# Performance work log

Hardware: AMD Instinct MI355X
Metric: run time of the kernel (lower is better)

The kernel has to match this reference:

```python
import jax, jax.numpy as jnp
import numpy as np

DIST_THR = 0.2
CONTACT_TGT = 0.1
ALPHA = 0.01
HUBER_DELTA = 0.01
W_BCE = 0.5
W_DIST = 1.0
EPS = 1e-06


def setup_inputs() -> dict:
    key = jax.random.key(0)
    k1, k2, k3, k4 = jax.random.split(key, 4)
    BT, Vh, Vo = 16, 6890, 2048
    return {
        "human_verts": jax.random.uniform(k1, (BT, Vh, 3), dtype=jnp.float32),
        "object_verts": jax.random.uniform(k2, (BT, Vo, 3), dtype=jnp.float32),
        "gt_human_verts": jax.random.uniform(k3, (BT, Vh, 3), dtype=jnp.float32),
        "gt_object_verts": jax.random.uniform(k4, (BT, Vo, 3), dtype=jnp.float32),
    }


def _min_cdist(A, B):
    # A:[BT,NA,3], B:[BT,NB,3] -> min Euclidean distance over B: [BT,NA]
    aa = jnp.sum(A * A, axis=-1)               # [BT,NA]
    bb = jnp.sum(B * B, axis=-1)               # [BT,NB]
    ab = jnp.einsum("bnd,bmd->bnm", A, B)      # [BT,NA,NB]
    d2 = aa[:, :, None] + bb[:, None, :] - 2.0 * ab
    d = jnp.sqrt(jnp.maximum(d2, 0.0))
    return jnp.min(d, axis=-1)


def _bce_balanced(p, target):
    p = jnp.clip(p, 1e-06, 1.0 - 1e-06)
    pos = jnp.sum(target)
    neg = target.size - pos
    pos_w = (neg + EPS) / (pos + EPS)
    w = jnp.where(target > 0.5, pos_w, 1.0)
    loss = -(target * jnp.log(p) + (1.0 - target) * jnp.log(1.0 - p))
    return jnp.mean(w * loss)


def _masked_huber(over, mask):
    m = (mask > 0.5).astype(over.dtype)
    ax = jnp.abs(over)
    hub = jnp.where(ax < HUBER_DELTA, 0.5 * ax * ax / HUBER_DELTA, ax - 0.5 * HUBER_DELTA)
    cnt = jnp.sum(m)
    s = jnp.sum(hub * m)
    return jnp.where(cnt > 0, s / jnp.maximum(cnt, 1.0), 0.0)


def reference(human_verts, object_verts, gt_human_verts, gt_object_verts):
    dmin_h = _min_cdist(human_verts, object_verts)      # [BT,Vh]
    dmin_o = _min_cdist(object_verts, human_verts)      # [BT,Vo]
    dmin_h_gt = _min_cdist(gt_human_verts, gt_object_verts)
    dmin_o_gt = _min_cdist(gt_object_verts, gt_human_verts)
    gt_mask_h = (dmin_h_gt < DIST_THR).astype(jnp.float32)
    gt_mask_o = (dmin_o_gt < DIST_THR).astype(jnp.float32)

    inv_alpha = 1.0 / max(ALPHA, 1e-08)
    p_h = jax.nn.sigmoid((DIST_THR - dmin_h) * inv_alpha)
    p_o = jax.nn.sigmoid((DIST_THR - dmin_o) * inv_alpha)
    L_bce = 0.5 * (_bce_balanced(p_h, gt_mask_h) + _bce_balanced(p_o, gt_mask_o))

    over_h = jnp.maximum(dmin_h - CONTACT_TGT, 0.0)
    over_o = jnp.maximum(dmin_o - CONTACT_TGT, 0.0)
    L_dist = _masked_huber(over_h, gt_mask_h) + _masked_huber(over_o, gt_mask_o)

    return W_BCE * L_bce + W_DIST * L_dist
```

## Files before the change

kernel.cpp:

```cpp
#include <hip/hip_runtime.h>
#include <math.h>


#define BT 16
#define VH 6890
#define VO 2048
#define NH (BT * VH)
#define NO (BT * VO)
#define RBLK1 54
#define RBLK2 16
#define NT1 64
#define NT2 216
#define NPROB 32
#define NBLK1 (NPROB * RBLK1)
#define NBLK2 (NPROB * RBLK2)

typedef __attribute__((ext_vector_type(8))) short          short8;
typedef __attribute__((ext_vector_type(8))) unsigned short ushort8;

__device__ __forceinline__ unsigned short bf16_rne(float f) {
    const unsigned int u = __float_as_uint(f);
    return (unsigned short)((u + 0x7FFFu + ((u >> 16) & 1u)) >> 16);
}
__device__ __forceinline__ float bf16_tof(unsigned short h) {
    return __uint_as_float(((unsigned int)h) << 16);
}

#define CLOB_B0 "v40","v41","v42","v43","v44","v45","v46","v47", \
                "v48","v49","v50","v51","v52","v53","v54","v55", \
                "v56","v57","v58","v59","v60","v61","v62","v63", \
                "v64","v65","v66","v67","v68","v69","v70","v71"
#define CLOB_B1 "v72","v73","v74","v75","v76","v77","v78","v79", \
                "v80","v81","v82","v83","v84","v85","v86","v87", \
                "v88","v89","v90","v91","v92","v93","v94","v95", \
                "v96","v97","v98","v99","v100","v101","v102","v103"

#define MFMA_B0(b0, b1) \
    asm volatile("v_mfma_f32_32x32x16_bf16 v[40:55], %0, %1, 0\n\t" \
                 "v_mfma_f32_32x32x16_bf16 v[56:71], %0, %2, 0" \
                 :: "v"(a8), "v"(b0), "v"(b1) : CLOB_B0)
#define MFMA_B1(b0, b1) \
    asm volatile("v_mfma_f32_32x32x16_bf16 v[72:87], %0, %1, 0\n\t" \
                 "v_mfma_f32_32x32x16_bf16 v[88:103], %0, %2, 0" \
                 :: "v"(a8), "v"(b0), "v"(b1) : CLOB_B1)

#define RED_B0() \
    asm volatile( \
        "v_min3_f32 %0, %0, v40, v56\n\t"  "v_min3_f32 %1, %1, v41, v57\n\t" \
        "v_min3_f32 %2, %2, v42, v58\n\t"  "v_min3_f32 %3, %3, v43, v59\n\t" \
        "v_min3_f32 %4, %4, v44, v60\n\t"  "v_min3_f32 %5, %5, v45, v61\n\t" \
        "v_min3_f32 %6, %6, v46, v62\n\t"  "v_min3_f32 %7, %7, v47, v63\n\t" \
        "v_min3_f32 %8, %8, v48, v64\n\t"  "v_min3_f32 %9, %9, v49, v65\n\t" \
        "v_min3_f32 %10, %10, v50, v66\n\t" "v_min3_f32 %11, %11, v51, v67\n\t" \
        "v_min3_f32 %12, %12, v52, v68\n\t" "v_min3_f32 %13, %13, v53, v69\n\t" \
        "v_min3_f32 %14, %14, v54, v70\n\t" "v_min3_f32 %15, %15, v55, v71" \
        : "+v"(rm[0]), "+v"(rm[1]), "+v"(rm[2]),  "+v"(rm[3]), \
          "+v"(rm[4]), "+v"(rm[5]), "+v"(rm[6]),  "+v"(rm[7]), \
          "+v"(rm[8]), "+v"(rm[9]), "+v"(rm[10]), "+v"(rm[11]), \
          "+v"(rm[12]),"+v"(rm[13]),"+v"(rm[14]), "+v"(rm[15]))
#define RED_B1() \
    asm volatile( \
        "v_min3_f32 %0, %0, v72, v88\n\t"  "v_min3_f32 %1, %1, v73, v89\n\t" \
        "v_min3_f32 %2, %2, v74, v90\n\t"  "v_min3_f32 %3, %3, v75, v91\n\t" \
        "v_min3_f32 %4, %4, v76, v92\n\t"  "v_min3_f32 %5, %5, v77, v93\n\t" \
        "v_min3_f32 %6, %6, v78, v94\n\t"  "v_min3_f32 %7, %7, v79, v95\n\t" \
        "v_min3_f32 %8, %8, v80, v96\n\t"  "v_min3_f32 %9, %9, v81, v97\n\t" \
        "v_min3_f32 %10, %10, v82, v98\n\t" "v_min3_f32 %11, %11, v83, v99\n\t" \
        "v_min3_f32 %12, %12, v84, v100\n\t" "v_min3_f32 %13, %13, v85, v101\n\t" \
        "v_min3_f32 %14, %14, v86, v102\n\t" "v_min3_f32 %15, %15, v87, v103" \
        : "+v"(rm[0]), "+v"(rm[1]), "+v"(rm[2]),  "+v"(rm[3]), \
          "+v"(rm[4]), "+v"(rm[5]), "+v"(rm[6]),  "+v"(rm[7]), \
          "+v"(rm[8]), "+v"(rm[9]), "+v"(rm[10]), "+v"(rm[11]), \
          "+v"(rm[12]),"+v"(rm[13]),"+v"(rm[14]), "+v"(rm[15]))

__global__ __launch_bounds__(256)
void prep_kernel(const float* __restrict__ hv,  const float* __restrict__ ov,
                 const float* __restrict__ ghv, const float* __restrict__ gov,
                 unsigned short* __restrict__ BfragO, unsigned short* __restrict__ BfragH,
                 unsigned int* __restrict__ acc)
{
    const int t = blockIdx.x * 256 + threadIdx.x;
    if (t < 16) acc[t] = 0u;

    const unsigned short one = 0x3F80;
    if (t < 65536) {
        const int col = t & 2047;
        const int bt  = (t >> 11) & 15;
        const int pg  = t >> 15;
        const float* B = (pg ? gov : ov) + ((size_t)bt * VO + col) * 3;
        const float bx = B[0], by = B[1], bz = B[2];
        const float m2x = -2.f * bx, m2y = -2.f * by, m2z = -2.f * bz;
        const float bb  = fmaf(bx, bx, fmaf(by, by, bz * bz));
        const unsigned short hx = bf16_rne(m2x), hy = bf16_rne(m2y), hz = bf16_rne(m2z);
        const unsigned short lx = bf16_rne(m2x - bf16_tof(hx));
        const unsigned short ly = bf16_rne(m2y - bf16_tof(hy));
        const unsigned short lz = bf16_rne(m2z - bf16_tof(hz));
        const unsigned short bh = bf16_rne(bb);
        const unsigned short bl = bf16_rne(bb - bf16_tof(bh));
        const int prob = pg * 16 + bt;
        unsigned short* d0 = BfragO +
            ((size_t)((prob * NT1 + (col >> 5)) * 64 + (col & 31))) * 8;
        const ushort8 w0 = {hx, hy, hz, hx, hy, hz, one, one};
        const ushort8 w1 = {lx, ly, lz, lx, ly, lz, bh, bl};
        *(ushort8*)d0         = w0;
        *(ushort8*)(d0 + 256) = w1;
    } else {
        const int t2   = t - 65536;
        const int col  = t2 % 6912;
        const int prob = t2 / 6912;
        const int pg = prob >> 4, bt = prob & 15;
        ushort8 w0, w1;
        if (col < VH) {
            const float* B = (pg ? ghv : hv) + ((size_t)bt * VH + col) * 3;
            const float bx = B[0], by = B[1], bz = B[2];
            const float m2x = -2.f * bx, m2y = -2.f * by, m2z = -2.f * bz;
            const float bb  = fmaf(bx, bx, fmaf(by, by, bz * bz));
            const unsigned short hx = bf16_rne(m2x), hy = bf16_rne(m2y), hz = bf16_rne(m2z);
            const unsigned short lx = bf16_rne(m2x - bf16_tof(hx));
            const unsigned short ly = bf16_rne(m2y - bf16_tof(hy));
            const unsigned short lz = bf16_rne(m2z - bf16_tof(hz));
            const unsigned short bh = bf16_rne(bb);
            const unsigned short bl = bf16_rne(bb - bf16_tof(bh));
            w0 = (ushort8){hx, hy, hz, hx, hy, hz, one, one};
            w1 = (ushort8){lx, ly, lz, lx, ly, lz, bh, bl};
        } else {
            const unsigned short big = bf16_rne(1.0e36f);
            w0 = (ushort8){0, 0, 0, 0, 0, 0, one, one};
            w1 = (ushort8){0, 0, 0, 0, 0, 0, big, 0};
        }
        unsigned short* d0 = BfragH +
            ((size_t)((prob * NT2 + (col >> 5)) * 64 + (col & 31))) * 8;
        *(ushort8*)d0         = w0;
        *(ushort8*)(d0 + 256) = w1;
    }
}

__global__ __launch_bounds__(256)
void mindist_mfma(const float* __restrict__ hv,  const float* __restrict__ ov,
                  const float* __restrict__ ghv, const float* __restrict__ gov,
                  const unsigned short* __restrict__ BfragO,
                  const unsigned short* __restrict__ BfragH,
                  float* __restrict__ rowm,
                  float* __restrict__ objm)
{
    const int tid  = threadIdx.x;
    const int lane = tid & 63;
    const int wave = tid >> 6;
    const int b    = blockIdx.x;

    const float* A;
    const short8* bls;
    float* out;
    int pairs, nA, row0;

    if (b < NBLK1) {
        const int prob = b / RBLK1, rblk = b - prob * RBLK1;
        const int pg = prob >> 4, bt = prob & 15;
        A    = (pg ? ghv : hv) + (size_t)bt * VH * 3;
        bls  = (const short8*)BfragO + (size_t)prob * (NT1 * 64);
        out  = rowm + (size_t)prob * VH;
        pairs = NT1 / 2; nA = VH; row0 = rblk * 128 + wave * 32;
    } else {
        const int b2 = b - NBLK1;
        const int prob = b2 >> 4, rblk = b2 & 15;
        const int pg = prob >> 4, bt = prob & 15;
        A    = (pg ? gov : ov) + (size_t)bt * VO * 3;
        bls  = (const short8*)BfragH + (size_t)prob * (NT2 * 64);
        out  = objm + (size_t)prob * 2048;
        pairs = NT2 / 2; nA = VO; row0 = rblk * 128 + wave * 32;
    }

    const int r = row0 + (lane & 31);
    float x, y, z;
    if (r < nA) { x = A[3*r]; y = A[3*r+1]; z = A[3*r+2]; }
    else        { x = 1.0e4f; y = 0.f;      z = 0.f; }
    const float aa = fmaf(x, x, fmaf(y, y, z * z));
    const unsigned short ahx = bf16_rne(x), ahy = bf16_rne(y), ahz = bf16_rne(z);
    const unsigned short alx = bf16_rne(x - bf16_tof(ahx));
    const unsigned short aly = bf16_rne(y - bf16_tof(ahy));
    const unsigned short alz = bf16_rne(z - bf16_tof(ahz));
    const unsigned short aah = bf16_rne(aa);
    const unsigned short aal = bf16_rne(aa - bf16_tof(aah));
    const int g = lane >> 5;
    ushort8 a8u;
    a8u[0] = ahx; a8u[1] = ahy; a8u[2] = ahz;
    a8u[3] = alx; a8u[4] = aly; a8u[5] = alz;
    a8u[6] = g ? (unsigned short)0x3F80 : aah;
    a8u[7] = g ? (unsigned short)0x3F80 : aal;
    const short8 a8 = (short8)a8u;

#define LD(jt) bls[(jt) * 64 + lane]
    float rm[16];
#pragma unroll
    for (int i = 0; i < 16; ++i) rm[i] = 3.0e38f;

    short8 bE0 = LD(0), bE1 = LD(1);
    MFMA_B0(bE0, bE1);
    short8 bO0 = LD(2), bO1 = LD(3);

    for (int s = 1; s < pairs - 1; s += 2) {
        bE0 = LD(2*s + 2); bE1 = LD(2*s + 3);
        MFMA_B1(bO0, bO1);
        RED_B0();
        bO0 = LD(2*s + 4); bO1 = LD(2*s + 5);
        MFMA_B0(bE0, bE1);
        RED_B1();
    }
    MFMA_B1(bO0, bO1);
    RED_B0();
    asm volatile("s_nop 7\n\ts_nop 7");
    RED_B1();
#undef LD

#pragma unroll
    for (int i = 0; i < 16; ++i) {
        float v = rm[i];
        v = fminf(v, __shfl_xor(v, 1));
        v = fminf(v, __shfl_xor(v, 2));
        v = fminf(v, __shfl_xor(v, 4));
        v = fminf(v, __shfl_xor(v, 8));
        v = fminf(v, __shfl_xor(v, 16));
        rm[i] = v;
    }
    if ((lane & 31) == 0) {
#pragma unroll
        for (int i = 0; i < 16; ++i) {
            const int rr = row0 + (i & 3) + 8 * (i >> 2) + 4 * g;
            if (rr < nA) out[rr] = fmaxf(rm[i], 0.f);
        }
    }
}

#define NBLK_H 431
#define NBLK_O 128
#define NBLKR  (NBLK_H + NBLK_O)

__global__ __launch_bounds__(256)
void reduce_kernel(const float* __restrict__ rowm, const float* __restrict__ objm,
                   float* __restrict__ acc)
{
    const int b = blockIdx.x;
    float p2 = 3.0e38f, g2 = 3.0e38f;
    float* a4;
    bool valid;

    if (b < NBLK_H) {
        a4 = acc;
        const int i = b * 256 + threadIdx.x;
        valid = (i < NH);
        if (valid) {
            const int bt = i / VH;
            const int r  = i - bt * VH;
            p2 = rowm[(size_t)bt * VH + r];
            g2 = rowm[(size_t)(16 + bt) * VH + r];
        }
    } else {
        a4 = acc + 4;
        const int i = (b - NBLK_H) * 256 + threadIdx.x;
        valid = true;
        const int bt = i >> 11;
        const int j  = i & 2047;
        p2 = objm[(size_t)bt * 2048 + j];
        g2 = objm[(size_t)(16 + bt) * 2048 + j];
    }

    float t = 0.f, sp = 0.f, sn = 0.f, sh = 0.f;
    if (valid) {
        const float d  = sqrtf(p2);
        const float dg = sqrtf(g2);
        const float tt = (dg < 0.2f) ? 1.f : 0.f;

        const float z = (0.2f - d) * 100.0f;
        float p = 1.0f / (1.0f + expf(-z));
        p = fminf(fmaxf(p, 1e-6f), 1.0f - 1e-6f);
        const float bce = (tt > 0.5f) ? -logf(p) : -logf(1.0f - p);

        const float over = fmaxf(d - 0.1f, 0.0f);
        const float hub  = (over < 0.01f) ? (0.5f * over * over) / 0.01f
                                          : (over - 0.5f * 0.01f);
        t  = tt;
        sp = tt * bce;
        sn = (1.0f - tt) * bce;
        sh = tt * hub;
    }
    for (int off = 32; off > 0; off >>= 1) {
        t  += __shfl_down(t,  off);
        sp += __shfl_down(sp, off);
        sn += __shfl_down(sn, off);
        sh += __shfl_down(sh, off);
    }
    __shared__ float wsum[4][4];
    const int wid = threadIdx.x >> 6, lane = threadIdx.x & 63;
    if (lane == 0) {
        wsum[wid][0] = t; wsum[wid][1] = sp; wsum[wid][2] = sn; wsum[wid][3] = sh;
    }
    __syncthreads();
    if (threadIdx.x == 0) {
        float s0 = 0, s1 = 0, s2 = 0, s3 = 0;
        for (int w = 0; w < 4; ++w) {
            s0 += wsum[w][0]; s1 += wsum[w][1]; s2 += wsum[w][2]; s3 += wsum[w][3];
        }
        atomicAdd(&a4[0], s0);
        atomicAdd(&a4[1], s1);
        atomicAdd(&a4[2], s2);
        atomicAdd(&a4[3], s3);
    }
}

__global__ void finalize_kernel(const float* __restrict__ acc, float* __restrict__ outp)
{
    const float Ph = acc[0], SpH = acc[1], SnH = acc[2], ShH = acc[3];
    const float Po = acc[4], SpO = acc[5], SnO = acc[6], ShO = acc[7];
    const float Nh = (float)NH, No = (float)NO;

    const float pwH = ((Nh - Ph) + 1e-6f) / (Ph + 1e-6f);
    const float pwO = ((No - Po) + 1e-6f) / (Po + 1e-6f);
    const float bceH = (pwH * SpH + SnH) / Nh;
    const float bceO = (pwO * SpO + SnO) / No;
    const float Lbce = 0.5f * (bceH + bceO);

    const float LdH = (Ph > 0.f) ? ShH / fmaxf(Ph, 1.f) : 0.f;
    const float LdO = (Po > 0.f) ? ShO / fmaxf(Po, 1.f) : 0.f;

    outp[0] = 0.5f * Lbce + (LdH + LdO);
}

extern "C" void kernel_launch(void* const* d_in, const int* in_sizes, int n_in,
                              void* d_out, int out_size, void* d_ws, size_t ws_size,
                              hipStream_t stream)
{
    const float* hv  = (const float*)d_in[0];
    const float* ov  = (const float*)d_in[1];
    const float* ghv = (const float*)d_in[2];
    const float* gov = (const float*)d_in[3];

    unsigned short* BfragO = (unsigned short*)d_ws;
    unsigned short* BfragH = BfragO + (size_t)NPROB * NT1 * 64 * 8;
    float*          rowm   = (float*)(BfragH + (size_t)NPROB * NT2 * 64 * 8);
    float*          objm   = rowm + (size_t)NPROB * VH;
    float*          acc    = objm + (size_t)NPROB * 2048;

    prep_kernel<<<1120, 256, 0, stream>>>(hv, ov, ghv, gov, BfragO, BfragH,
                                          (unsigned int*)acc);

    mindist_mfma<<<NBLK1 + NBLK2, 256, 0, stream>>>(hv, ov, ghv, gov,
                                                    BfragO, BfragH, rowm, objm);

    reduce_kernel<<<NBLKR, 256, 0, stream>>>(rowm, objm, acc);

    finalize_kernel<<<1, 1, 0, stream>>>(acc, (float*)d_out);
}
```

Before: 139.5 us.

## Deepen B-fragment prefetch to four pairs and interleave block-to-problem mapping

The MFMA main loop now keeps four pairs of B fragments in flight instead of two, so global loads are issued further ahead of their use. This is meant to hide load latency that the two-deep pipeline left exposed. Block indices are also remapped so that consecutive blocks cycle across 8 problems instead of staying in one, which changes how work and memory traffic spread across CUs and caches. The deeper prefetch adds register pressure, and the loop's tail assumes the pair count is a multiple of 4 (32 and 108 both are).

```diff
diff --git a/kernel.cpp b/kernel.cpp
--- a/kernel.cpp
+++ b/kernel.cpp
@@ -154,7 +154,9 @@
     int pairs, nA, row0;
 
     if (b < NBLK1) {
-        const int prob = b / RBLK1, rblk = b - prob * RBLK1;
+        const int x = b & 7, y = b >> 3;
+        const int q = y / RBLK1, rblk = y - q * RBLK1;
+        const int prob = x + 8 * q;
         const int pg = prob >> 4, bt = prob & 15;
         A    = (pg ? ghv : hv) + (size_t)bt * VH * 3;
         bls  = (const short8*)BfragO + (size_t)prob * (NT1 * 64);
@@ -162,7 +164,9 @@
         pairs = NT1 / 2; nA = VH; row0 = rblk * 128 + wave * 32;
     } else {
         const int b2 = b - NBLK1;
-        const int prob = b2 >> 4, rblk = b2 & 15;
+        const int x = b2 & 7, y = b2 >> 3;
+        const int q = y >> 4, rblk = y & 15;
+        const int prob = x + 8 * q;
         const int pg = prob >> 4, bt = prob & 15;
         A    = (pg ? gov : ov) + (size_t)bt * VO * 3;
         bls  = (const short8*)BfragH + (size_t)prob * (NT2 * 64);
@@ -189,28 +193,33 @@
     a8u[7] = g ? (unsigned short)0x3F80 : aal;
     const short8 a8 = (short8)a8u;
 
-#define LD(jt) bls[(jt) * 64 + lane]
+#define LDT(jt) bls[(jt) * 64 + lane]
     float rm[16];
 #pragma unroll
     for (int i = 0; i < 16; ++i) rm[i] = 3.0e38f;
 
-    short8 bE0 = LD(0), bE1 = LD(1);
-    MFMA_B0(bE0, bE1);
-    short8 bO0 = LD(2), bO1 = LD(3);
-
-    for (int s = 1; s < pairs - 1; s += 2) {
-        bE0 = LD(2*s + 2); bE1 = LD(2*s + 3);
-        MFMA_B1(bO0, bO1);
-        RED_B0();
-        bO0 = LD(2*s + 4); bO1 = LD(2*s + 5);
-        MFMA_B0(bE0, bE1);
-        RED_B1();
-    }
-    MFMA_B1(bO0, bO1);
-    RED_B0();
+    short8 bAl = LDT(0), bAh = LDT(1);
+    short8 bBl = LDT(2), bBh = LDT(3);
+    short8 bCl = LDT(4), bCh = LDT(5);
+    short8 bDl = LDT(6), bDh = LDT(7);
+    MFMA_B0(bAl, bAh);
+
+    for (int p = 0; p + 8 <= pairs; p += 4) {
+        bAl = LDT(2*(p+4)); bAh = LDT(2*(p+4)+1);
+        MFMA_B1(bBl, bBh);  RED_B0();
+        bBl = LDT(2*(p+5)); bBh = LDT(2*(p+5)+1);
+        MFMA_B0(bCl, bCh);  RED_B1();
+        bCl = LDT(2*(p+6)); bCh = LDT(2*(p+6)+1);
+        MFMA_B1(bDl, bDh);  RED_B0();
+        bDl = LDT(2*(p+7)); bDh = LDT(2*(p+7)+1);
+        MFMA_B0(bAl, bAh);  RED_B1();
+    }
+    MFMA_B1(bBl, bBh);  RED_B0();
+    MFMA_B0(bCl, bCh);  RED_B1();
+    MFMA_B1(bDl, bDh);  RED_B0();
     asm volatile("s_nop 7\n\ts_nop 7");
     RED_B1();
-#undef LD
+#undef LDT
 
 #pragma unroll
     for (int i = 0; i < 16; ++i) {
```

New measurement: 134.7 us. 3.4% less time.
